# Kernel tuning notes

Measured on AMD Instinct MI355X. Metric: run time of the kernel, lower is better.

Reference implementation:

```python
import jax, jax.numpy as jnp
from jax import lax
import numpy as np

B, N, C = 8, 16384, 64
NPOINT, NSAMPLE, RADIUS = 1024, 32, 0.2


def setup_inputs() -> dict:
    key = jax.random.key(0)
    ks = jax.random.split(key, 6)
    xyz = jax.random.normal(ks[0], (B, N, 3), jnp.float32)
    features = jax.random.normal(ks[1], (B, C, N), jnp.float32)
    W1 = jax.random.normal(ks[2], (64, C + 3), jnp.float32) * 0.1
    b1 = jnp.zeros((64,), jnp.float32)
    W2 = jax.random.normal(ks[3], (64, 64), jnp.float32) * 0.1
    b2 = jnp.zeros((64,), jnp.float32)
    W3 = jax.random.normal(ks[4], (128, 64), jnp.float32) * 0.1
    b3 = jnp.zeros((128,), jnp.float32)
    return {"xyz": xyz, "features": features, "W1": W1, "b1": b1,
            "W2": W2, "b2": b2, "W3": W3, "b3": b3}


def furthest_point_sample(xyz, npoint):
    # Iterative FPS: start at index 0, greedily pick farthest point. (B,N,3) -> (B,npoint) int32
    b, n, _ = xyz.shape

    def body(carry, _):
        dist, last = carry  # dist: (B,N) min sq-dist to chosen set; last: (B,) last chosen idx
        lastpt = jnp.take_along_axis(xyz, last[:, None, None], axis=1)  # (B,1,3)
        d = jnp.sum((xyz - lastpt) ** 2, axis=-1)
        dist = jnp.minimum(dist, d)
        nxt = jnp.argmax(dist, axis=1).astype(jnp.int32)
        return (dist, nxt), nxt

    init = (jnp.full((b, n), 1e10, xyz.dtype), jnp.zeros((b,), jnp.int32))
    _, idxs = lax.scan(body, init, None, length=npoint - 1)  # (npoint-1, B)
    return jnp.concatenate([jnp.zeros((1, b), jnp.int32), idxs], axis=0).T  # (B,npoint)


def ball_query(xyz, new_xyz, radius, nsample):
    # For each centroid, take first (lowest-index) nsample points within radius,
    # padding with the first found neighbor (matches CUDA ball_query semantics).
    n = xyz.shape[1]
    d2 = jnp.sum((new_xyz[:, :, None, :] - xyz[:, None, :, :]) ** 2, axis=-1)  # (B,S,N)
    within = d2 <= radius * radius
    order = jnp.where(within, jnp.arange(n, dtype=jnp.int32), n)
    idx = -lax.top_k(-order, nsample)[0]  # smallest indices first, (B,S,nsample)
    first = idx[..., :1]
    idx = jnp.where(idx < n, idx, first)  # pad slots with first neighbor
    count = jnp.minimum(jnp.sum(within, axis=-1), nsample)  # (B,S)
    return idx, count


def reference(xyz, features, W1, b1, W2, b2, W3, b3):
    b = xyz.shape[0]
    fps_idx = furthest_point_sample(xyz, NPOINT)            # (B,S)
    bi = jnp.arange(b)[:, None]
    new_xyz = xyz[bi, fps_idx]                              # (B,S,3)
    idx, count = ball_query(xyz, new_xyz, RADIUS, NSAMPLE)  # (B,S,ns)
    bi3 = jnp.arange(b)[:, None, None]
    grouped_xyz = xyz[bi3, idx] - new_xyz[:, :, None, :]    # (B,S,ns,3) relative coords
    grouped_feat = features.transpose(0, 2, 1)[bi3, idx]    # (B,S,ns,C)
    grouped = jnp.concatenate([grouped_xyz, grouped_feat], axis=-1).transpose(0, 3, 1, 2)  # (B,3+C,S,ns)
    # Shared MLP (1x1 conv + ReLU stack)
    h = jax.nn.relu(jnp.einsum('oc,bcsn->bosn', W1, grouped) + b1[None, :, None, None])
    h = jax.nn.relu(jnp.einsum('oc,bcsn->bosn', W2, h) + b2[None, :, None, None])
    h = jax.nn.relu(jnp.einsum('oc,bcsn->bosn', W3, h) + b3[None, :, None, None])
    new_features = jnp.max(h, axis=-1)                      # max pool over neighbors -> (B,128,S)
    return new_xyz, new_features
```

## Files before the change

### kernel.cpp

```cpp
#include <hip/hip_runtime.h>

#define BQ 8
#define NPTS 16384
#define CFEAT 64
#define NPOINT 1024
#define NSAMPLE 32
#define RADIUS2 0.04f

typedef float v2f __attribute__((ext_vector_type(2)));

template <int CTRL, int RMASK>
__device__ __forceinline__ void dpp_max3(unsigned& hi, unsigned& lo, float& zz) {
  unsigned ohi = (unsigned)__builtin_amdgcn_update_dpp((int)hi, (int)hi, CTRL, RMASK, 0xf, false);
  unsigned olo = (unsigned)__builtin_amdgcn_update_dpp((int)lo, (int)lo, CTRL, RMASK, 0xf, false);
  int oz = __builtin_amdgcn_update_dpp(__float_as_int(zz), __float_as_int(zz), CTRL, RMASK, 0xf, false);
  unsigned long long ok = (((unsigned long long)ohi) << 32) | olo;
  unsigned long long ck = (((unsigned long long)hi) << 32) | lo;
  if (ok > ck) { hi = ohi; lo = olo; zz = __int_as_float(oz); }
}

__global__ __launch_bounds__(1024, 4) void fused_front_kernel(
    const float* __restrict__ xyz, const float* __restrict__ feat,
    const float* __restrict__ W1, const float* __restrict__ W2,
    const float* __restrict__ W3, float* __restrict__ WT,
    float* __restrict__ featT, float* __restrict__ newxyz) {
  __shared__ __align__(16) char raw[131072];
  __shared__ uint4 s_tab[2][16];
  const int blk = blockIdx.x;
  const int t = threadIdx.x;

  if (blk < 8) {
#pragma clang fp contract(off)
    const int b = blk;
    const float* xb = xyz + (size_t)b * NPTS * 3;
    float* nb = newxyz + (size_t)b * NPOINT * 3;
    float* sx = (float*)raw;
    float* sy = (float*)(raw + 65536);
    v2f* sx2 = (v2f*)sx;
    v2f* sy2 = (v2f*)sy;
    v2f zc[8], dd[8];
#pragma unroll
    for (int k = 0; k < 8; ++k) {
      const int p0 = (k << 11) | (t << 1);
      v2f xv, yv, zv, d0;
      xv.x = xb[p0 * 3 + 0]; xv.y = xb[p0 * 3 + 3];
      yv.x = xb[p0 * 3 + 1]; yv.y = xb[p0 * 3 + 4];
      zv.x = xb[p0 * 3 + 2]; zv.y = xb[p0 * 3 + 5];
      d0.x = 1e10f; d0.y = 1e10f;
      sx2[(k << 10) | t] = xv;
      sy2[(k << 10) | t] = yv;
      zc[k] = zv;
      dd[k] = d0;
    }
    float wx = xb[0], wy = xb[1], wz = xb[2];
    if (t == 0) { nb[0] = wx; nb[1] = wy; nb[2] = wz; }
    const int w = t >> 6;
    const int lane = t & 63;
    __syncthreads();
    for (int j = 1; j < NPOINT; ++j) {
      v2f lx2, ly2, lz2;
      lx2.x = wx; lx2.y = wx;
      ly2.x = wy; ly2.y = wy;
      lz2.x = wz; lz2.y = wz;
      float bestv = -1.0f, bestz = 0.0f;
      int bestK = 0;
#pragma unroll
      for (int k = 0; k < 8; ++k) {
        v2f xv = sx2[(k << 10) | t];
        v2f yv = sy2[(k << 10) | t];
        v2f dx = xv - lx2;
        v2f dy = yv - ly2;
        v2f dz = zc[k] - lz2;
        v2f sxx = dx * dx;
        v2f syy = dy * dy;
        v2f sxy = sxx + syy;
        v2f szz = dz * dz;
        v2f d = sxy + szz;
        float n0 = fminf(dd[k].x, d.x);
        float n1 = fminf(dd[k].y, d.y);
        v2f nd; nd.x = n0; nd.y = n1;
        dd[k] = nd;
        if (n0 > bestv) { bestv = n0; bestK = 2 * k; bestz = zc[k].x; }
        if (n1 > bestv) { bestv = n1; bestK = 2 * k + 1; bestz = zc[k].y; }
      }
      const int gidx = ((bestK >> 1) << 11) | (t << 1) | (bestK & 1);
      unsigned hi = __float_as_uint(bestv);
      unsigned lo = (unsigned)(16384 - gidx);
      float bz = bestz;
      dpp_max3<0x111, 0xf>(hi, lo, bz);
      dpp_max3<0x112, 0xf>(hi, lo, bz);
      dpp_max3<0x114, 0xf>(hi, lo, bz);
      dpp_max3<0x118, 0xf>(hi, lo, bz);
      dpp_max3<0x142, 0xa>(hi, lo, bz);
      dpp_max3<0x143, 0xc>(hi, lo, bz);
      const int pw = j & 1;
      if (lane == 63) {
        uint4 e; e.x = hi; e.y = lo; e.z = __float_as_uint(bz); e.w = 0;
        s_tab[pw][w] = e;
      }
      __syncthreads();
      uint4 e = s_tab[pw][lane & 15];
      unsigned hi2 = e.x, lo2 = e.y;
      float z2 = __uint_as_float(e.z);
      dpp_max3<0x111, 0xf>(hi2, lo2, z2);
      dpp_max3<0x112, 0xf>(hi2, lo2, z2);
      dpp_max3<0x114, 0xf>(hi2, lo2, z2);
      dpp_max3<0x118, 0xf>(hi2, lo2, z2);
      const int wlo = __builtin_amdgcn_readlane((int)lo2, 15);
      wz = __int_as_float(__builtin_amdgcn_readlane(__float_as_int(z2), 15));
      const int wi = 16384 - wlo;
      wx = sx[wi];
      wy = sy[wi];
      if (t == 0) { float* o = nb + j * 3; o[0] = wx; o[1] = wy; o[2] = wz; }
    }
  } else if (blk == 8) {
    float* W1T = WT;
    float* W2T = WT + 67 * 64;
    float* W3T = WT + 67 * 64 + 64 * 64;
    for (int i = t; i < 64 * 67; i += 1024) { int o = i / 67, c = i - o * 67; W1T[c * 64 + o] = W1[i]; }
    for (int i = t; i < 64 * 64; i += 1024) { int o = i >> 6, c = i & 63; W2T[c * 64 + o] = W2[i]; }
    for (int i = t; i < 128 * 64; i += 1024) { int o = i >> 6, c = i & 63; W3T[c * 128 + o] = W3[i]; }
  } else {
    float (*tile)[129] = (float(*)[129])raw;
    const int tid = blk - 9;
    const int b = tid >> 7;
    const int n0 = (tid & 127) << 7;
    const int col = t & 127;
    const int row = t >> 7;
#pragma unroll
    for (int k = 0; k < 8; ++k) {
      int c = k * 8 + row;
      tile[c][col] = feat[((size_t)b * CFEAT + c) * NPTS + n0 + col];
    }
    __syncthreads();
    const int cc = t & 63;
#pragma unroll
    for (int k = 0; k < 8; ++k) {
      int nl = (t >> 6) + 16 * k;
      featT[((size_t)b * NPTS + n0 + nl) * CFEAT + cc] = tile[cc][nl];
    }
  }
}

__global__ __launch_bounds__(256) void ballquery_kernel(const float* __restrict__ xyz,
                                                        const float* __restrict__ newxyz,
                                                        int* __restrict__ idxout) {
#pragma clang fp contract(off)
  const int blk = blockIdx.x;
  const int b = blk >> 8;
  const int t = threadIdx.x;
  const int w = t >> 6;
  const int lane = t & 63;
  const int q = ((blk & 255) << 2) | w;
  const int g = b * NPOINT + q;
  const float* xb = xyz + (size_t)b * NPTS * 3;
  const float qx = newxyz[(size_t)g * 3 + 0];
  const float qy = newxyz[(size_t)g * 3 + 1];
  const float qz = newxyz[(size_t)g * 3 + 2];
  __shared__ __align__(16) float lds[2048 * 3];
  int total = 0;
  int first = 0;
  const unsigned long long ltmask = (1ull << lane) - 1ull;
  for (int T = 0; T < 8; ++T) {
    __syncthreads();
    const float4* src = (const float4*)(xb + (size_t)T * 2048 * 3);
#pragma unroll
    for (int k = 0; k < 6; ++k) ((float4*)lds)[t + 256 * k] = src[t + 256 * k];
    __syncthreads();
    if (total < NSAMPLE) {
      for (int c = 0; c < 32; ++c) {
        const int il = (c << 6) | lane;
        float dx = lds[il * 3 + 0] - qx;
        float dy = lds[il * 3 + 1] - qy;
        float dz = lds[il * 3 + 2] - qz;
        float d2 = dx * dx + dy * dy;
        d2 = d2 + dz * dz;
        const bool within = d2 <= RADIUS2;
        const unsigned long long mask = __ballot(within);
        if (total == 0 && mask != 0ull)
          first = (T << 11) | (c << 6) | (__ffsll((unsigned long long)mask) - 1);
        if (within) {
          int pos = total + __popcll(mask & ltmask);
          if (pos < NSAMPLE) idxout[(size_t)g * NSAMPLE + pos] = (T << 11) | il;
        }
        total += __popcll(mask);
        if (total >= NSAMPLE) break;
      }
    }
  }
  if (total < NSAMPLE) {
    if (lane >= total && lane < NSAMPLE) idxout[(size_t)g * NSAMPLE + lane] = first;
  }
}

template <bool USE_FEATT>
__global__ __launch_bounds__(256) void mlp_kernel(const float* __restrict__ xyz,
                                                  const float* __restrict__ feat,
                                                  const float* __restrict__ featT,
                                                  const float* __restrict__ newxyz,
                                                  const int* __restrict__ idx,
                                                  const float* __restrict__ WT,
                                                  const float* __restrict__ b1,
                                                  const float* __restrict__ b2,
                                                  const float* __restrict__ b3,
                                                  float* __restrict__ outfeat) {
  const int g = blockIdx.x;
  const int b = g >> 10;
  const int q = g & 1023;
  const int t = threadIdx.x;
  const int s = t >> 3;
  const int u = t & 7;
  __shared__ float in_s[32][69];
  __shared__ float h1_s[32][69];
  __shared__ float h2_s[32][69];
  __shared__ float h3_s[32][132];
  const float* W1T = WT;
  const float* W2T = WT + 67 * 64;
  const float* W3T = WT + 67 * 64 + 64 * 64;

  const int gi = idx[(size_t)g * NSAMPLE + s];
  if (u == 0) {
    const float* p = xyz + ((size_t)b * NPTS + gi) * 3;
    const float* c = newxyz + (size_t)g * 3;
    in_s[s][0] = p[0] - c[0];
    in_s[s][1] = p[1] - c[1];
    in_s[s][2] = p[2] - c[2];
  }
  if (USE_FEATT) {
    const float* fr = featT + ((size_t)b * NPTS + gi) * CFEAT + u * 8;
    float4 a = *(const float4*)fr;
    float4 c4 = *(const float4*)(fr + 4);
    in_s[s][3 + u * 8 + 0] = a.x;  in_s[s][3 + u * 8 + 1] = a.y;
    in_s[s][3 + u * 8 + 2] = a.z;  in_s[s][3 + u * 8 + 3] = a.w;
    in_s[s][3 + u * 8 + 4] = c4.x; in_s[s][3 + u * 8 + 5] = c4.y;
    in_s[s][3 + u * 8 + 6] = c4.z; in_s[s][3 + u * 8 + 7] = c4.w;
  } else {
#pragma unroll
    for (int k = 0; k < 8; ++k)
      in_s[s][3 + u * 8 + k] = feat[((size_t)b * CFEAT + u * 8 + k) * NPTS + gi];
  }
  __syncthreads();
  {
    float acc[8];
    const int o0 = u * 8;
#pragma unroll
    for (int k = 0; k < 8; ++k) acc[k] = b1[o0 + k];
    for (int c = 0; c < 67; ++c) {
      float x = in_s[s][c];
      const float* wp = W1T + c * 64 + o0;
      float4 w0 = *(const float4*)wp;
      float4 w1 = *(const float4*)(wp + 4);
      acc[0] += w0.x * x; acc[1] += w0.y * x; acc[2] += w0.z * x; acc[3] += w0.w * x;
      acc[4] += w1.x * x; acc[5] += w1.y * x; acc[6] += w1.z * x; acc[7] += w1.w * x;
    }
#pragma unroll
    for (int k = 0; k < 8; ++k) h1_s[s][o0 + k] = fmaxf(acc[k], 0.0f);
  }
  __syncthreads();
  {
    float acc[8];
    const int o0 = u * 8;
#pragma unroll
    for (int k = 0; k < 8; ++k) acc[k] = b2[o0 + k];
    for (int c = 0; c < 64; ++c) {
      float x = h1_s[s][c];
      const float* wp = W2T + c * 64 + o0;
      float4 w0 = *(const float4*)wp;
      float4 w1 = *(const float4*)(wp + 4);
      acc[0] += w0.x * x; acc[1] += w0.y * x; acc[2] += w0.z * x; acc[3] += w0.w * x;
      acc[4] += w1.x * x; acc[5] += w1.y * x; acc[6] += w1.z * x; acc[7] += w1.w * x;
    }
#pragma unroll
    for (int k = 0; k < 8; ++k) h2_s[s][o0 + k] = fmaxf(acc[k], 0.0f);
  }
  __syncthreads();
  {
    float acc[16];
    const int o0 = u * 16;
#pragma unroll
    for (int k = 0; k < 16; ++k) acc[k] = b3[o0 + k];
    for (int c = 0; c < 64; ++c) {
      float x = h2_s[s][c];
      const float* wp = W3T + c * 128 + o0;
      float4 w0 = *(const float4*)wp;
      float4 w1 = *(const float4*)(wp + 4);
      float4 w2 = *(const float4*)(wp + 8);
      float4 w3 = *(const float4*)(wp + 12);
      acc[0] += w0.x * x;  acc[1] += w0.y * x;  acc[2] += w0.z * x;  acc[3] += w0.w * x;
      acc[4] += w1.x * x;  acc[5] += w1.y * x;  acc[6] += w1.z * x;  acc[7] += w1.w * x;
      acc[8] += w2.x * x;  acc[9] += w2.y * x;  acc[10] += w2.z * x; acc[11] += w2.w * x;
      acc[12] += w3.x * x; acc[13] += w3.y * x; acc[14] += w3.z * x; acc[15] += w3.w * x;
    }
#pragma unroll
    for (int k = 0; k < 16; ++k) h3_s[s][o0 + k] = fmaxf(acc[k], 0.0f);
  }
  __syncthreads();
  if (t < 128) {
    float m = h3_s[0][t];
#pragma unroll 4
    for (int ss = 1; ss < 32; ++ss) m = fmaxf(m, h3_s[ss][t]);
    outfeat[((size_t)b * 128 + t) * NPOINT + q] = m;
  }
}

extern "C" void kernel_launch(void* const* d_in, const int* in_sizes, int n_in,
                              void* d_out, int out_size, void* d_ws, size_t ws_size,
                              hipStream_t stream) {
  const float* xyz = (const float*)d_in[0];
  const float* features = (const float*)d_in[1];
  const float* W1 = (const float*)d_in[2];
  const float* b1 = (const float*)d_in[3];
  const float* W2 = (const float*)d_in[4];
  const float* b2 = (const float*)d_in[5];
  const float* W3 = (const float*)d_in[6];
  const float* b3 = (const float*)d_in[7];
  float* out_newxyz = (float*)d_out;
  float* out_feat = (float*)d_out + (size_t)BQ * NPOINT * 3;

  char* ws = (char*)d_ws;
  int* idx = (int*)ws;
  float* WT = (float*)(ws + (1 << 20));
  float* featT = (float*)(ws + (1 << 20) + 66560);
  const size_t need = (size_t)(1 << 20) + 66560 + (size_t)BQ * NPTS * CFEAT * 4;
  const bool useT = ws_size >= need;

  const int nfront = useT ? (9 + (NPTS / 128) * BQ) : 9;
  hipLaunchKernelGGL(fused_front_kernel, dim3(nfront), dim3(1024), 0, stream,
                     xyz, features, W1, W2, W3, WT, featT, out_newxyz);
  hipLaunchKernelGGL(ballquery_kernel, dim3(BQ * NPOINT / 4), dim3(256), 0, stream,
                     xyz, out_newxyz, idx);
  if (useT)
    hipLaunchKernelGGL(mlp_kernel<true>, dim3(BQ * NPOINT), dim3(256), 0, stream,
                       xyz, features, featT, out_newxyz, idx, WT, b1, b2, b3, out_feat);
  else
    hipLaunchKernelGGL(mlp_kernel<false>, dim3(BQ * NPOINT), dim3(256), 0, stream,
                       xyz, features, featT, out_newxyz, idx, WT, b1, b2, b3, out_feat);
}
```

Baseline: 2.938 ms.

## Halve FPS block to 512 threads and pack argmax key into doubles

The furthest-point-sampling block now uses 512 threads with 16 point pairs per thread, so the cross-wave reduction goes from 16 waves to 8 and the barrier covers fewer waves. The per-thread argmax uses fmax over doubles built from (distance bits, inverted index) instead of branchy compares, and the z coordinate is no longer carried through the DPP reduction. The winner's z is instead reloaded from global memory, which adds a dependent global load to every serial iteration. The feature-transpose blocks are resized to 64-point tiles to match the new block size.

Result: faster. 2.576 ms (-12.3%).

```diff
diff --git a/kernel.cpp b/kernel.cpp
--- a/kernel.cpp
+++ b/kernel.cpp
@@ -10,22 +10,21 @@
 typedef float v2f __attribute__((ext_vector_type(2)));
 
 template <int CTRL, int RMASK>
-__device__ __forceinline__ void dpp_max3(unsigned& hi, unsigned& lo, float& zz) {
+__device__ __forceinline__ void dpp_max2(unsigned& hi, unsigned& lo) {
   unsigned ohi = (unsigned)__builtin_amdgcn_update_dpp((int)hi, (int)hi, CTRL, RMASK, 0xf, false);
   unsigned olo = (unsigned)__builtin_amdgcn_update_dpp((int)lo, (int)lo, CTRL, RMASK, 0xf, false);
-  int oz = __builtin_amdgcn_update_dpp(__float_as_int(zz), __float_as_int(zz), CTRL, RMASK, 0xf, false);
   unsigned long long ok = (((unsigned long long)ohi) << 32) | olo;
   unsigned long long ck = (((unsigned long long)hi) << 32) | lo;
-  if (ok > ck) { hi = ohi; lo = olo; zz = __int_as_float(oz); }
-}
-
-__global__ __launch_bounds__(1024, 4) void fused_front_kernel(
+  if (ok > ck) { hi = ohi; lo = olo; }
+}
+
+__global__ __launch_bounds__(512, 1) void fused_front_kernel(
     const float* __restrict__ xyz, const float* __restrict__ feat,
     const float* __restrict__ W1, const float* __restrict__ W2,
     const float* __restrict__ W3, float* __restrict__ WT,
     float* __restrict__ featT, float* __restrict__ newxyz) {
   __shared__ __align__(16) char raw[131072];
-  __shared__ uint4 s_tab[2][16];
+  __shared__ uint2 s_tab[2][8];
   const int blk = blockIdx.x;
   const int t = threadIdx.x;
 
@@ -38,17 +37,19 @@
     float* sy = (float*)(raw + 65536);
     v2f* sx2 = (v2f*)sx;
     v2f* sy2 = (v2f*)sy;
-    v2f zc[8], dd[8];
-#pragma unroll
-    for (int k = 0; k < 8; ++k) {
-      const int p0 = (k << 11) | (t << 1);
+    v2f zc[16], dd[16];
+#pragma unroll
+    for (int k = 0; k < 16; ++k) {
+      const int pi = (k << 9) | t;
+      const v2f* pp = (const v2f*)(xb + (size_t)(pi << 1) * 3);
+      v2f a = pp[0], bb = pp[1], c = pp[2];
       v2f xv, yv, zv, d0;
-      xv.x = xb[p0 * 3 + 0]; xv.y = xb[p0 * 3 + 3];
-      yv.x = xb[p0 * 3 + 1]; yv.y = xb[p0 * 3 + 4];
-      zv.x = xb[p0 * 3 + 2]; zv.y = xb[p0 * 3 + 5];
+      xv.x = a.x;  xv.y = bb.y;
+      yv.x = a.y;  yv.y = c.x;
+      zv.x = bb.x; zv.y = c.y;
       d0.x = 1e10f; d0.y = 1e10f;
-      sx2[(k << 10) | t] = xv;
-      sy2[(k << 10) | t] = yv;
+      sx2[pi] = xv;
+      sy2[pi] = yv;
       zc[k] = zv;
       dd[k] = d0;
     }
@@ -62,53 +63,48 @@
       lx2.x = wx; lx2.y = wx;
       ly2.x = wy; ly2.y = wy;
       lz2.x = wz; lz2.y = wz;
-      float bestv = -1.0f, bestz = 0.0f;
-      int bestK = 0;
-#pragma unroll
-      for (int k = 0; k < 8; ++k) {
-        v2f xv = sx2[(k << 10) | t];
-        v2f yv = sy2[(k << 10) | t];
+      double best = -1.0;
+#pragma unroll
+      for (int k = 0; k < 16; ++k) {
+        v2f xv = sx2[(k << 9) | t];
+        v2f yv = sy2[(k << 9) | t];
         v2f dx = xv - lx2;
         v2f dy = yv - ly2;
         v2f dz = zc[k] - lz2;
-        v2f sxx = dx * dx;
-        v2f syy = dy * dy;
-        v2f sxy = sxx + syy;
-        v2f szz = dz * dz;
-        v2f d = sxy + szz;
+        v2f s1 = dx * dx;
+        v2f s2 = dy * dy;
+        v2f s3 = s1 + s2;
+        v2f s4 = dz * dz;
+        v2f d = s3 + s4;
         float n0 = fminf(dd[k].x, d.x);
         float n1 = fminf(dd[k].y, d.y);
         v2f nd; nd.x = n0; nd.y = n1;
         dd[k] = nd;
-        if (n0 > bestv) { bestv = n0; bestK = 2 * k; bestz = zc[k].x; }
-        if (n1 > bestv) { bestv = n1; bestK = 2 * k + 1; bestz = zc[k].y; }
+        const int i0 = (k << 10) | (t << 1);
+        double c0 = __hiloint2double(__float_as_int(n0), 16384 - i0);
+        double c1 = __hiloint2double(__float_as_int(n1), 16383 - i0);
+        best = fmax(best, c0);
+        best = fmax(best, c1);
       }
-      const int gidx = ((bestK >> 1) << 11) | (t << 1) | (bestK & 1);
-      unsigned hi = __float_as_uint(bestv);
-      unsigned lo = (unsigned)(16384 - gidx);
-      float bz = bestz;
-      dpp_max3<0x111, 0xf>(hi, lo, bz);
-      dpp_max3<0x112, 0xf>(hi, lo, bz);
-      dpp_max3<0x114, 0xf>(hi, lo, bz);
-      dpp_max3<0x118, 0xf>(hi, lo, bz);
-      dpp_max3<0x142, 0xa>(hi, lo, bz);
-      dpp_max3<0x143, 0xc>(hi, lo, bz);
+      unsigned hi = (unsigned)__double2hiint(best);
+      unsigned lo = (unsigned)__double2loint(best);
+      dpp_max2<0x111, 0xf>(hi, lo);
+      dpp_max2<0x112, 0xf>(hi, lo);
+      dpp_max2<0x114, 0xf>(hi, lo);
+      dpp_max2<0x118, 0xf>(hi, lo);
+      dpp_max2<0x142, 0xa>(hi, lo);
+      dpp_max2<0x143, 0xc>(hi, lo);
       const int pw = j & 1;
-      if (lane == 63) {
-        uint4 e; e.x = hi; e.y = lo; e.z = __float_as_uint(bz); e.w = 0;
-        s_tab[pw][w] = e;
-      }
+      if (lane == 63) { uint2 e; e.x = hi; e.y = lo; s_tab[pw][w] = e; }
       __syncthreads();
-      uint4 e = s_tab[pw][lane & 15];
+      uint2 e = s_tab[pw][lane & 7];
       unsigned hi2 = e.x, lo2 = e.y;
-      float z2 = __uint_as_float(e.z);
-      dpp_max3<0x111, 0xf>(hi2, lo2, z2);
-      dpp_max3<0x112, 0xf>(hi2, lo2, z2);
-      dpp_max3<0x114, 0xf>(hi2, lo2, z2);
-      dpp_max3<0x118, 0xf>(hi2, lo2, z2);
-      const int wlo = __builtin_amdgcn_readlane((int)lo2, 15);
-      wz = __int_as_float(__builtin_amdgcn_readlane(__float_as_int(z2), 15));
+      dpp_max2<0x111, 0xf>(hi2, lo2);
+      dpp_max2<0x112, 0xf>(hi2, lo2);
+      dpp_max2<0x114, 0xf>(hi2, lo2);
+      const int wlo = __builtin_amdgcn_readlane((int)lo2, 7);
       const int wi = 16384 - wlo;
+      wz = xb[(size_t)wi * 3 + 2];
       wx = sx[wi];
       wy = sy[wi];
       if (t == 0) { float* o = nb + j * 3; o[0] = wx; o[1] = wy; o[2] = wz; }
@@ -117,27 +113,26 @@
     float* W1T = WT;
     float* W2T = WT + 67 * 64;
     float* W3T = WT + 67 * 64 + 64 * 64;
-    for (int i = t; i < 64 * 67; i += 1024) { int o = i / 67, c = i - o * 67; W1T[c * 64 + o] = W1[i]; }
-    for (int i = t; i < 64 * 64; i += 1024) { int o = i >> 6, c = i & 63; W2T[c * 64 + o] = W2[i]; }
-    for (int i = t; i < 128 * 64; i += 1024) { int o = i >> 6, c = i & 63; W3T[c * 128 + o] = W3[i]; }
+    for (int i = t; i < 64 * 67; i += 512) { int o = i / 67, c = i - o * 67; W1T[c * 64 + o] = W1[i]; }
+    for (int i = t; i < 64 * 64; i += 512) { int o = i >> 6, c = i & 63; W2T[c * 64 + o] = W2[i]; }
+    for (int i = t; i < 128 * 64; i += 512) { int o = i >> 6, c = i & 63; W3T[c * 128 + o] = W3[i]; }
   } else {
-    float (*tile)[129] = (float(*)[129])raw;
+    float (*tile)[65] = (float(*)[65])raw;
     const int tid = blk - 9;
-    const int b = tid >> 7;
-    const int n0 = (tid & 127) << 7;
-    const int col = t & 127;
-    const int row = t >> 7;
+    const int b = tid >> 8;
+    const int n0 = (tid & 255) << 6;
+    const int col = t & 63;
+    const int row = t >> 6;
 #pragma unroll
     for (int k = 0; k < 8; ++k) {
       int c = k * 8 + row;
       tile[c][col] = feat[((size_t)b * CFEAT + c) * NPTS + n0 + col];
     }
     __syncthreads();
-    const int cc = t & 63;
 #pragma unroll
     for (int k = 0; k < 8; ++k) {
-      int nl = (t >> 6) + 16 * k;
-      featT[((size_t)b * NPTS + n0 + nl) * CFEAT + cc] = tile[cc][nl];
+      int nl = k * 8 + row;
+      featT[((size_t)b * NPTS + n0 + nl) * CFEAT + col] = tile[col][nl];
     }
   }
 }
@@ -324,8 +319,8 @@
   const size_t need = (size_t)(1 << 20) + 66560 + (size_t)BQ * NPTS * CFEAT * 4;
   const bool useT = ws_size >= need;
 
-  const int nfront = useT ? (9 + (NPTS / 128) * BQ) : 9;
-  hipLaunchKernelGGL(fused_front_kernel, dim3(nfront), dim3(1024), 0, stream,
+  const int nfront = useT ? (9 + (NPTS / 64) * BQ) : 9;
+  hipLaunchKernelGGL(fused_front_kernel, dim3(nfront), dim3(512), 0, stream,
                      xyz, features, W1, W2, W3, WT, featT, out_newxyz);
   hipLaunchKernelGGL(ballquery_kernel, dim3(BQ * NPOINT / 4), dim3(256), 0, stream,
                      xyz, out_newxyz, idx);
```
